# Kernel tuning notes

Measured on AMD Instinct MI355X. Metric: run time of the kernel, lower is better.

The kernel has to match this reference:

```python
import jax, jax.numpy as jnp
import numpy as np

NUM_BINS = 256          # CLAHE histogram bins (kornia default)
GRID = (8, 8)           # CLAHE tile grid (kornia default)
LOG_GAIN = 2.5          # module init arg
CLIP_LIMIT = 1.0        # module init arg


def normalize_in_range(x, lo=0.0, hi=1.0):
    mn = x.min()
    mx = x.max()
    return (x - mn) / (mx - mn) * (hi - lo) + lo


def adjust_log(x, gain):
    # skimage/kornia log adjust: gain * log2(1 + x)
    return gain * jnp.log2(1.0 + x)


def equalize_clahe(x, clip_limit=CLIP_LIMIT, grid=GRID):
    B, C, H, W = x.shape
    gh, gw = grid
    th = -(-H // gh)   # ceil tile height
    tw = -(-W // gw)   # ceil tile width
    Hp, Wp = th * gh, tw * gw
    if (Hp, Wp) != (H, W):
        x = jnp.pad(x, ((0, 0), (0, 0), (0, Hp - H), (0, Wp - W)), mode='reflect')

    # bin index per pixel (values saturated into [0,1])
    xc = jnp.clip(x, 0.0, 1.0)
    bins = jnp.clip((xc * NUM_BINS).astype(jnp.int32), 0, NUM_BINS - 1)  # B,C,Hp,Wp

    # --- per-tile histograms: (B*C*gh*gw) tiles of th*tw pixels ---
    tb = bins.reshape(B, C, gh, th, gw, tw).transpose(0, 1, 2, 4, 3, 5)
    tb = tb.reshape(B * C * gh * gw, th * tw)
    hist = jax.vmap(lambda ix: jnp.bincount(ix, length=NUM_BINS))(tb).astype(jnp.float32)

    pixels = th * tw
    # --- clip + uniform redistribution of excess ---
    if clip_limit > 0:
        clip_max = max(int(clip_limit * pixels // NUM_BINS), 1)
        excess = jnp.maximum(hist - clip_max, 0.0).sum(-1)
        hist = jnp.minimum(hist, float(clip_max))
        redist = jnp.floor(excess / NUM_BINS)
        residual = excess - redist * NUM_BINS
        hist = hist + redist[:, None] \
             + (jnp.arange(NUM_BINS)[None, :] < residual[:, None]).astype(hist.dtype)

    # --- CDF -> LUT in [0, 255] ---
    lut = jnp.clip(jnp.floor(jnp.cumsum(hist, -1) * ((NUM_BINS - 1) / pixels)), 0.0, NUM_BINS - 1.0)
    lut = lut.reshape(B, C, gh, gw, NUM_BINS)

    # --- bilinear interpolation between the 4 neighboring tile LUTs ---
    iy = jnp.arange(Hp, dtype=jnp.float32)
    ty = (iy + 0.5) / th - 0.5
    y0f = jnp.floor(ty)
    wy = (ty - y0f)[:, None]                                   # Hp x 1
    y0 = jnp.clip(y0f.astype(jnp.int32), 0, gh - 1)[:, None]
    y1 = jnp.clip(y0f.astype(jnp.int32) + 1, 0, gh - 1)[:, None]

    ix = jnp.arange(Wp, dtype=jnp.float32)
    tx = (ix + 0.5) / tw - 0.5
    x0f = jnp.floor(tx)
    wx = (tx - x0f)[None, :]
    x0 = jnp.clip(x0f.astype(jnp.int32), 0, gw - 1)[None, :]
    x1 = jnp.clip(x0f.astype(jnp.int32) + 1, 0, gw - 1)[None, :]

    flat_lut = lut.reshape(-1)
    bidx = jnp.arange(B)[:, None, None, None]
    cidx = jnp.arange(C)[None, :, None, None]

    def gather(yi, xi):
        idx = (((bidx * C + cidx) * gh + yi) * gw + xi) * NUM_BINS + bins
        return flat_lut[idx]

    v = (1.0 - wy) * ((1.0 - wx) * gather(y0, x0) + wx * gather(y0, x1)) \
        + wy * ((1.0 - wx) * gather(y1, x0) + wx * gather(y1, x1))
    out = v / (NUM_BINS - 1)
    return out[..., :H, :W]


def setup_inputs() -> dict:
    key = jax.random.key(0)
    x = jax.random.uniform(key, (8, 1, 2048, 2048), dtype=jnp.float32)
    return {"x": x}


def reference(x):
    shape = x.shape
    x = normalize_in_range(x, 0.0, 1.0)
    x = adjust_log(x, gain=LOG_GAIN)
    x = equalize_clahe(x, clip_limit=CLIP_LIMIT)
    x = normalize_in_range(x, 0.0, 1.0)
    return x.reshape(shape)
```

## Files before the change

### kernel.cpp

```cpp
#include <hip/hip_runtime.h>

#define NIMG 8
#define IMH 2048
#define IMW 2048
#define GH 8
#define GW 8
#define NBINS 256
#define NTPI 64
#define CLIP_MAXF 256.0f
#define LUT_SCALE 0.0038909912109375f
#define LOG_GAIN_F 2.5f

#define MM_BLOCKS 2048
#define APPLY_BLOCKS (16 * 16 * NIMG)

__device__ __forceinline__ int pix_bin(float v, float mn, float den) {
    float xn = (v - mn) / den;
    float t  = LOG_GAIN_F * log2f(1.0f + xn);
    float xc = fminf(fmaxf(t, 0.0f), 1.0f);
    int b = (int)(xc * 256.0f);
    return min(max(b, 0), 255);
}

__device__ __forceinline__ void mm4(float4 v, float& mn, float& mx) {
    mn = fminf(mn, fminf(fminf(v.x, v.y), fminf(v.z, v.w)));
    mx = fmaxf(mx, fmaxf(fmaxf(v.x, v.y), fmaxf(v.z, v.w)));
}

template <int NWAVES>
__device__ __forceinline__ void block_minmax_all(float& mn, float& mx, int t) {
#pragma unroll
    for (int m = 32; m >= 1; m >>= 1) {
        mn = fminf(mn, __shfl_xor(mn, m, 64));
        mx = fmaxf(mx, __shfl_xor(mx, m, 64));
    }
    __shared__ float smn[NWAVES], smx[NWAVES];
    int wid = t >> 6, lid = t & 63;
    if (lid == 0) { smn[wid] = mn; smx[wid] = mx; }
    __syncthreads();
    mn = smn[0]; mx = smx[0];
#pragma unroll
    for (int i = 1; i < NWAVES; i++) { mn = fminf(mn, smn[i]); mx = fmaxf(mx, smx[i]); }
}

__global__ __launch_bounds__(256) void k_minmax_in(const float4* __restrict__ x,
                                                   float2* __restrict__ red) {
    int t = threadIdx.x;
    size_t base = (size_t)blockIdx.x * 4096 + t;
    float mn = 3.4e38f, mx = -3.4e38f;
#pragma unroll
    for (int k = 0; k < 16; k += 4) {
        float4 v0 = x[base + (size_t)(k + 0) * 256];
        float4 v1 = x[base + (size_t)(k + 1) * 256];
        float4 v2 = x[base + (size_t)(k + 2) * 256];
        float4 v3 = x[base + (size_t)(k + 3) * 256];
        mm4(v0, mn, mx); mm4(v1, mn, mx); mm4(v2, mn, mx); mm4(v3, mn, mx);
    }
    block_minmax_all<4>(mn, mx, t);
    if (t == 0) red[blockIdx.x] = make_float2(mn, mx);
}

__global__ __launch_bounds__(256) void k_reduce_minmax(const float2* __restrict__ red, int n,
                                                       float* __restrict__ sc, int slot) {
    int t = threadIdx.x;
    float mn = 3.4e38f, mx = -3.4e38f;
    for (int i = t; i < n; i += 256) {
        float2 p = red[i];
        mn = fminf(mn, p.x);
        mx = fmaxf(mx, p.y);
    }
    block_minmax_all<4>(mn, mx, t);
    if (t == 0) { sc[slot] = mn; sc[slot + 1] = mx; }
}

template <bool STOREBINS>
__global__ __launch_bounds__(1024) void k_hist(const float* __restrict__ x,
                                               const float2* __restrict__ red1,
                                               float* __restrict__ lut,
                                               uchar4* __restrict__ bins) {
    int t = threadIdx.x;

    float mn, mx;
    {
        float2 p0 = red1[t];
        float2 p1 = red1[t + 1024];
        mn = fminf(p0.x, p1.x);
        mx = fmaxf(p0.y, p1.y);
        block_minmax_all<16>(mn, mx, t);
    }
    float den = mx - mn;

    __shared__ unsigned sh[NBINS];
    if (t < NBINS) sh[t] = 0u;
    __syncthreads();

    int tile = blockIdx.x;
    int img  = blockIdx.y;
    int ty = tile >> 3, tx = tile & 7;

    size_t base = ((size_t)img * IMH + (size_t)ty * 256) * IMW + (size_t)tx * 256;
    const float* xt = x + base;
    int lid = t & 63;
    int rowoff = t >> 6;
    int c4 = t & 63;

    for (int it = 0; it < 16; ++it) {
        int r = (it << 4) + rowoff;
        float4 v = *(const float4*)(xt + (size_t)r * IMW + (c4 << 2));
        int b[4];
        b[0] = pix_bin(v.x, mn, den);
        b[1] = pix_bin(v.y, mn, den);
        b[2] = pix_bin(v.z, mn, den);
        b[3] = pix_bin(v.w, mn, den);
#pragma unroll
        for (int j = 0; j < 4; j++) {
            bool hot = (b[j] == 255);
            unsigned long long m = __ballot(hot);
            if (!hot) atomicAdd(&sh[b[j]], 1u);
            if (lid == 0 && m) atomicAdd(&sh[255], (unsigned)__popcll(m));
        }
        if (STOREBINS) {
            uchar4 q;
            q.x = (unsigned char)b[0]; q.y = (unsigned char)b[1];
            q.z = (unsigned char)b[2]; q.w = (unsigned char)b[3];
            bins[(base + (size_t)r * IMW + (size_t)(c4 << 2)) >> 2] = q;
        }
    }
    __syncthreads();

    int wid = t >> 6;
    float h = 0.0f, ex = 0.0f;
    if (t < NBINS) {
        h = (float)sh[t];
        ex = fmaxf(h - CLIP_MAXF, 0.0f);
    }
    float s = ex;
#pragma unroll
    for (int m = 1; m < 64; m <<= 1) s += __shfl_xor(s, m, 64);
    __shared__ float wpart[16];
    if (lid == 0) wpart[wid] = s;
    __syncthreads();
    float excess = wpart[0] + wpart[1] + wpart[2] + wpart[3];

    h = fminf(h, CLIP_MAXF);
    float redist   = floorf(excess * (1.0f / 256.0f));
    float residual = excess - redist * 256.0f;
    h = h + redist + (((float)t < residual) ? 1.0f : 0.0f);

    float c = h;
#pragma unroll
    for (int m = 1; m < 64; m <<= 1) {
        float o = __shfl_up(c, m, 64);
        if (lid >= m) c += o;
    }
    __shared__ float wsum[16];
    if (lid == 63) wsum[wid] = c;
    __syncthreads();
    if (t < NBINS) {
        float off = 0.0f;
        for (int i = 0; i < wid; i++) off += wsum[i];
        c += off;
        float l = fminf(floorf(c * LUT_SCALE), 255.0f);
        l = fmaxf(l, 0.0f);
        lut[((size_t)img * NTPI + tile) * NBINS + t] = l;
    }
}

template <bool USE_BINS, bool FINAL>
__global__ __launch_bounds__(256) void k_apply(const uchar4* __restrict__ bins,
                                               const float* __restrict__ x,
                                               const float* __restrict__ lut,
                                               const float* __restrict__ sc,
                                               float2* __restrict__ red2,
                                               float4* __restrict__ out) {
    __shared__ float L[4][NBINS];
    int t = threadIdx.x;

    float pmn = 0.f, oscale = 1.f;
    if (FINAL) {
        float vmn = 3.4e38f, vmx = -3.4e38f;
#pragma unroll
        for (int k = 0; k < 8; k++) {
            float2 p = red2[t + k * 256];
            vmn = fminf(vmn, p.x);
            vmx = fmaxf(vmx, p.y);
        }
        block_minmax_all<4>(vmn, vmx, t);
        pmn = vmn * (1.0f / 255.0f);
        float pmx = vmx * (1.0f / 255.0f);
        oscale = 1.0f / (pmx - pmn);
    }

    int qx = blockIdx.x, qy = blockIdx.y, img = blockIdx.z;
    int ty = qy >> 1, tx = qx >> 1;
    int yA = (qy & 1) ? ty : max(ty - 1, 0);
    int yB = (qy & 1) ? min(ty + 1, GH - 1) : ty;
    int xA = (qx & 1) ? tx : max(tx - 1, 0);
    int xB = (qx & 1) ? min(tx + 1, GW - 1) : tx;

    const float* lb = lut + (size_t)img * NTPI * NBINS;
    L[0][t] = lb[(size_t)(yA * GW + xA) * NBINS + t];
    L[1][t] = lb[(size_t)(yA * GW + xB) * NBINS + t];
    L[2][t] = lb[(size_t)(yB * GW + xA) * NBINS + t];
    L[3][t] = lb[(size_t)(yB * GW + xB) * NBINS + t];
    __syncthreads();

    float mn = 0.f, den = 1.f;
    if (!USE_BINS) { mn = sc[0]; den = sc[1] - mn; }

    float vmnl = 3.4e38f, vmxl = -3.4e38f;
    int gy0 = qy << 7, gx0 = qx << 7;
    int rowoff = t >> 5;
    int c4 = t & 31;

    for (int it = 0; it < 16; ++it) {
        int r = (it << 3) + rowoff;
        int iy = gy0 + r;
        int ix0 = gx0 + (c4 << 2);
        size_t pidx = ((size_t)img * IMH + iy) * IMW + ix0;

        int b[4];
        if (USE_BINS) {
            uchar4 q = bins[pidx >> 2];
            b[0] = q.x; b[1] = q.y; b[2] = q.z; b[3] = q.w;
        } else {
            float4 v = *(const float4*)(x + pidx);
            b[0] = pix_bin(v.x, mn, den);
            b[1] = pix_bin(v.y, mn, den);
            b[2] = pix_bin(v.z, mn, den);
            b[3] = pix_bin(v.w, mn, den);
        }

        float tyf = ((float)iy + 0.5f) * (1.0f / 256.0f) - 0.5f;
        float wy = tyf - floorf(tyf);
        float4 o;
        float* op = &o.x;
#pragma unroll
        for (int j = 0; j < 4; j++) {
            float txf = ((float)(ix0 + j) + 0.5f) * (1.0f / 256.0f) - 0.5f;
            float wx = txf - floorf(txf);
            float g00 = L[0][b[j]], g01 = L[1][b[j]];
            float g10 = L[2][b[j]], g11 = L[3][b[j]];
            float v = (1.0f - wy) * ((1.0f - wx) * g00 + wx * g01) +
                      wy * ((1.0f - wx) * g10 + wx * g11);
            if (FINAL) {
                float p = v * (1.0f / 255.0f);
                op[j] = (p - pmn) * oscale;
            } else {
                vmnl = fminf(vmnl, v);
                vmxl = fmaxf(vmxl, v);
            }
        }
        if (FINAL) out[pidx >> 2] = o;
    }

    if (!FINAL) {
        block_minmax_all<4>(vmnl, vmxl, t);
        if (t == 0) {
            int bid = (img * 16 + qy) * 16 + qx;
            red2[bid] = make_float2(vmnl, vmxl);
        }
    }
}

extern "C" void kernel_launch(void* const* d_in, const int* in_sizes, int n_in,
                              void* d_out, int out_size, void* d_ws, size_t ws_size,
                              hipStream_t stream) {
    const float* x = (const float*)d_in[0];
    float4* out = (float4*)d_out;

    unsigned char* ws = (unsigned char*)d_ws;
    float* sc     = (float*)ws;
    float* lut    = (float*)(ws + 64);
    float2* red1  = (float2*)(ws + 64 + 512 * 1024);
    float2* red2  = (float2*)(ws + 64 + 512 * 1024 + 16384);
    uchar4* bins  = (uchar4*)(ws + 1024 * 1024);

    size_t need_bins = 1024 * 1024 + (size_t)NIMG * IMH * IMW;
    bool use_bins = (ws_size >= need_bins);

    k_minmax_in<<<dim3(MM_BLOCKS), dim3(256), 0, stream>>>((const float4*)x, red1);

    dim3 qgrid(16, 16, NIMG);
    if (use_bins) {
        k_hist<true><<<dim3(NTPI, NIMG), dim3(1024), 0, stream>>>(x, red1, lut, bins);
        k_apply<true, false><<<qgrid, dim3(256), 0, stream>>>(bins, x, lut, sc, red2, out);
        k_apply<true, true><<<qgrid, dim3(256), 0, stream>>>(bins, x, lut, sc, red2, out);
    } else {
        k_reduce_minmax<<<dim3(1), dim3(256), 0, stream>>>(red1, MM_BLOCKS, sc, 0);
        k_hist<false><<<dim3(NTPI, NIMG), dim3(1024), 0, stream>>>(x, red1, lut, bins);
        k_apply<false, false><<<qgrid, dim3(256), 0, stream>>>(bins, x, lut, sc, red2, out);
        k_apply<false, true><<<qgrid, dim3(256), 0, stream>>>(bins, x, lut, sc, red2, out);
    }
}
```

Measured before the change: 121.4 us.

## Fuse CLAHE pipeline into one cooperative kernel with grid syncs and LDS bins

Replaces the four-kernel sequence (min/max, histogram+LUT, apply-minmax, apply-final) with one cooperative kernel of 512 blocks, one per tile, separated by grid-wide syncs. Each block keeps its tile's 256x256 bin indices in 64KB of shared memory, so the global bins buffer is neither written nor read twice and launch gaps disappear. In exchange it needs co-residency of all 512 blocks of 512 threads with 64KB+ LDS each, which may not fit and falls back to the multi-kernel path. The fallback's k_apply now loads L twice, with an out-of-range write when t>=256 in a 256-thread block.

```diff
diff --git a/kernel.cpp b/kernel.cpp
--- a/kernel.cpp
+++ b/kernel.cpp
@@ -1,4 +1,7 @@
 #include <hip/hip_runtime.h>
+#include <hip/hip_cooperative_groups.h>
+
+namespace cg = cooperative_groups;
 
 #define NIMG 8
 #define IMH 2048
@@ -11,8 +14,8 @@
 #define LUT_SCALE 0.0038909912109375f
 #define LOG_GAIN_F 2.5f
 
+#define FUSED_BLOCKS 512
 #define MM_BLOCKS 2048
-#define APPLY_BLOCKS (16 * 16 * NIMG)
 
 __device__ __forceinline__ int pix_bin(float v, float mn, float den) {
     float xn = (v - mn) / den;
@@ -29,12 +32,13 @@
 
 template <int NWAVES>
 __device__ __forceinline__ void block_minmax_all(float& mn, float& mx, int t) {
+    __shared__ float smn[NWAVES], smx[NWAVES];
+    __syncthreads();
 #pragma unroll
     for (int m = 32; m >= 1; m >>= 1) {
         mn = fminf(mn, __shfl_xor(mn, m, 64));
         mx = fmaxf(mx, __shfl_xor(mx, m, 64));
     }
-    __shared__ float smn[NWAVES], smx[NWAVES];
     int wid = t >> 6, lid = t & 63;
     if (lid == 0) { smn[wid] = mn; smx[wid] = mx; }
     __syncthreads();
@@ -42,6 +46,207 @@
 #pragma unroll
     for (int i = 1; i < NWAVES; i++) { mn = fminf(mn, smn[i]); mx = fmaxf(mx, smx[i]); }
 }
+
+__device__ __forceinline__ void load_L(const float* __restrict__ lb, int qy, int qx,
+                                       float (*L)[NBINS], int t) {
+    int ty = qy >> 1, tx = qx >> 1;
+    int yA = (qy & 1) ? ty : max(ty - 1, 0);
+    int yB = (qy & 1) ? min(ty + 1, GH - 1) : ty;
+    int xA = (qx & 1) ? tx : max(tx - 1, 0);
+    int xB = (qx & 1) ? min(tx + 1, GW - 1) : tx;
+    int ci = t & 255;
+#pragma unroll
+    for (int j = 0; j < 2; ++j) {
+        int which = (t >> 8) + 2 * j;
+        int yy = (which >= 2) ? yB : yA;
+        int xx = (which & 1) ? xB : xA;
+        L[which][ci] = lb[(size_t)(yy * GW + xx) * NBINS + ci];
+    }
+}
+
+__global__ __launch_bounds__(512, 4) void k_fused(const float* __restrict__ x,
+                                                  float2* __restrict__ red1,
+                                                  float2* __restrict__ red2,
+                                                  float* __restrict__ lutg,
+                                                  float4* __restrict__ out) {
+    cg::grid_group gridg = cg::this_grid();
+    __shared__ unsigned char binsL[256 * 256];
+    __shared__ float L[4][NBINS];
+    __shared__ unsigned sh[NBINS];
+
+    int t = threadIdx.x;
+    int bid = blockIdx.x;
+    int img = bid >> 6, tile = bid & 63;
+    int ty = tile >> 3, tx = tile & 7;
+
+    float mn = 3.4e38f, mx = -3.4e38f;
+    {
+        const float4* x4 = (const float4*)x;
+        size_t base = (size_t)bid * 16384 + t;
+#pragma unroll
+        for (int k = 0; k < 32; k += 4) {
+            float4 v0 = x4[base + (size_t)(k + 0) * 512];
+            float4 v1 = x4[base + (size_t)(k + 1) * 512];
+            float4 v2 = x4[base + (size_t)(k + 2) * 512];
+            float4 v3 = x4[base + (size_t)(k + 3) * 512];
+            mm4(v0, mn, mx); mm4(v1, mn, mx); mm4(v2, mn, mx); mm4(v3, mn, mx);
+        }
+        block_minmax_all<8>(mn, mx, t);
+        if (t == 0) red1[bid] = make_float2(mn, mx);
+    }
+    gridg.sync();
+
+    {
+        float2 p = red1[t];
+        mn = p.x; mx = p.y;
+        block_minmax_all<8>(mn, mx, t);
+    }
+    float den = mx - mn;
+
+    if (t < NBINS) sh[t] = 0u;
+    __syncthreads();
+
+    size_t tbase = ((size_t)img * IMH + (size_t)ty * 256) * IMW + (size_t)tx * 256;
+    int lid = t & 63;
+    {
+        int rowoff = t >> 6;
+        int c4 = t & 63;
+        for (int it = 0; it < 32; ++it) {
+            int r = (it << 3) + rowoff;
+            float4 v = *(const float4*)(x + tbase + (size_t)r * IMW + (c4 << 2));
+            int b[4];
+            b[0] = pix_bin(v.x, mn, den);
+            b[1] = pix_bin(v.y, mn, den);
+            b[2] = pix_bin(v.z, mn, den);
+            b[3] = pix_bin(v.w, mn, den);
+#pragma unroll
+            for (int j = 0; j < 4; j++) {
+                bool hot = (b[j] == 255);
+                unsigned long long m = __ballot(hot);
+                if (!hot) atomicAdd(&sh[b[j]], 1u);
+                if (lid == 0 && m) atomicAdd(&sh[255], (unsigned)__popcll(m));
+            }
+            uchar4 q;
+            q.x = (unsigned char)b[0]; q.y = (unsigned char)b[1];
+            q.z = (unsigned char)b[2]; q.w = (unsigned char)b[3];
+            ((uchar4*)binsL)[(r << 6) + c4] = q;
+        }
+    }
+    __syncthreads();
+
+    {
+        int wid = t >> 6;
+        float h = 0.0f, ex = 0.0f;
+        if (t < NBINS) {
+            h = (float)sh[t];
+            ex = fmaxf(h - CLIP_MAXF, 0.0f);
+        }
+        float s = ex;
+#pragma unroll
+        for (int m = 1; m < 64; m <<= 1) s += __shfl_xor(s, m, 64);
+        __shared__ float wpart[8];
+        if (lid == 0) wpart[wid] = s;
+        __syncthreads();
+        float excess = wpart[0] + wpart[1] + wpart[2] + wpart[3];
+
+        h = fminf(h, CLIP_MAXF);
+        float redist   = floorf(excess * (1.0f / 256.0f));
+        float residual = excess - redist * 256.0f;
+        h = h + redist + (((float)t < residual) ? 1.0f : 0.0f);
+
+        float c = h;
+#pragma unroll
+        for (int m = 1; m < 64; m <<= 1) {
+            float o = __shfl_up(c, m, 64);
+            if (lid >= m) c += o;
+        }
+        __shared__ float wsum[8];
+        if (lid == 63) wsum[wid] = c;
+        __syncthreads();
+        if (t < NBINS) {
+            float off = 0.0f;
+            for (int i = 0; i < wid; i++) off += wsum[i];
+            c += off;
+            float l = fminf(floorf(c * LUT_SCALE), 255.0f);
+            l = fmaxf(l, 0.0f);
+            lutg[((size_t)img * NTPI + tile) * NBINS + t] = l;
+        }
+    }
+    gridg.sync();
+
+    const float* lb = lutg + (size_t)img * NTPI * NBINS;
+    float vmn = 3.4e38f, vmx = -3.4e38f;
+    for (int q = 0; q < 4; ++q) {
+        int qy = (ty << 1) + (q >> 1), qx = (tx << 1) + (q & 1);
+        __syncthreads();
+        load_L(lb, qy, qx, L, t);
+        __syncthreads();
+        int ly0 = (q >> 1) << 7, lx0 = (q & 1) << 7;
+        int rowoff = t >> 5, col4 = t & 31;
+        for (int it = 0; it < 8; ++it) {
+            int r = (it << 4) + rowoff;
+            uchar4 qb = ((const uchar4*)binsL)[((ly0 + r) << 6) + (lx0 >> 2) + col4];
+            int iy = (ty << 8) + ly0 + r;
+            float tyf = ((float)iy + 0.5f) * (1.0f / 256.0f) - 0.5f;
+            float wy = tyf - floorf(tyf);
+            int ix0 = (tx << 8) + lx0 + (col4 << 2);
+            int b[4] = {qb.x, qb.y, qb.z, qb.w};
+#pragma unroll
+            for (int j = 0; j < 4; j++) {
+                float txf = ((float)(ix0 + j) + 0.5f) * (1.0f / 256.0f) - 0.5f;
+                float wx = txf - floorf(txf);
+                float v = (1.0f - wy) * ((1.0f - wx) * L[0][b[j]] + wx * L[1][b[j]]) +
+                          wy * ((1.0f - wx) * L[2][b[j]] + wx * L[3][b[j]]);
+                vmn = fminf(vmn, v);
+                vmx = fmaxf(vmx, v);
+            }
+        }
+    }
+    block_minmax_all<8>(vmn, vmx, t);
+    if (t == 0) red2[bid] = make_float2(vmn, vmx);
+    gridg.sync();
+
+    float pmn, oscale;
+    {
+        float2 p = red2[t];
+        float a = p.x, b2 = p.y;
+        block_minmax_all<8>(a, b2, t);
+        pmn = a * (1.0f / 255.0f);
+        float pmx = b2 * (1.0f / 255.0f);
+        oscale = 1.0f / (pmx - pmn);
+    }
+    for (int q = 0; q < 4; ++q) {
+        int qy = (ty << 1) + (q >> 1), qx = (tx << 1) + (q & 1);
+        __syncthreads();
+        load_L(lb, qy, qx, L, t);
+        __syncthreads();
+        int ly0 = (q >> 1) << 7, lx0 = (q & 1) << 7;
+        int rowoff = t >> 5, col4 = t & 31;
+        for (int it = 0; it < 8; ++it) {
+            int r = (it << 4) + rowoff;
+            uchar4 qb = ((const uchar4*)binsL)[((ly0 + r) << 6) + (lx0 >> 2) + col4];
+            int iy = (ty << 8) + ly0 + r;
+            float tyf = ((float)iy + 0.5f) * (1.0f / 256.0f) - 0.5f;
+            float wy = tyf - floorf(tyf);
+            int ix0 = (tx << 8) + lx0 + (col4 << 2);
+            int b[4] = {qb.x, qb.y, qb.z, qb.w};
+            float4 o;
+            float* op = &o.x;
+#pragma unroll
+            for (int j = 0; j < 4; j++) {
+                float txf = ((float)(ix0 + j) + 0.5f) * (1.0f / 256.0f) - 0.5f;
+                float wx = txf - floorf(txf);
+                float v = (1.0f - wy) * ((1.0f - wx) * L[0][b[j]] + wx * L[1][b[j]]) +
+                          wy * ((1.0f - wx) * L[2][b[j]] + wx * L[3][b[j]]);
+                float p = v * (1.0f / 255.0f);
+                op[j] = (p - pmn) * oscale;
+            }
+            size_t pidx = ((size_t)img * IMH + iy) * IMW + ix0;
+            out[pidx >> 2] = o;
+        }
+    }
+}
+
 
 __global__ __launch_bounds__(256) void k_minmax_in(const float4* __restrict__ x,
                                                    float2* __restrict__ red) {
@@ -60,26 +265,11 @@
     if (t == 0) red[blockIdx.x] = make_float2(mn, mx);
 }
 
-__global__ __launch_bounds__(256) void k_reduce_minmax(const float2* __restrict__ red, int n,
-                                                       float* __restrict__ sc, int slot) {
-    int t = threadIdx.x;
-    float mn = 3.4e38f, mx = -3.4e38f;
-    for (int i = t; i < n; i += 256) {
-        float2 p = red[i];
-        mn = fminf(mn, p.x);
-        mx = fmaxf(mx, p.y);
-    }
-    block_minmax_all<4>(mn, mx, t);
-    if (t == 0) { sc[slot] = mn; sc[slot + 1] = mx; }
-}
-
-template <bool STOREBINS>
 __global__ __launch_bounds__(1024) void k_hist(const float* __restrict__ x,
                                                const float2* __restrict__ red1,
                                                float* __restrict__ lut,
                                                uchar4* __restrict__ bins) {
     int t = threadIdx.x;
-
     float mn, mx;
     {
         float2 p0 = red1[t];
@@ -97,7 +287,6 @@
     int tile = blockIdx.x;
     int img  = blockIdx.y;
     int ty = tile >> 3, tx = tile & 7;
-
     size_t base = ((size_t)img * IMH + (size_t)ty * 256) * IMW + (size_t)tx * 256;
     const float* xt = x + base;
     int lid = t & 63;
@@ -119,12 +308,10 @@
             if (!hot) atomicAdd(&sh[b[j]], 1u);
             if (lid == 0 && m) atomicAdd(&sh[255], (unsigned)__popcll(m));
         }
-        if (STOREBINS) {
-            uchar4 q;
-            q.x = (unsigned char)b[0]; q.y = (unsigned char)b[1];
-            q.z = (unsigned char)b[2]; q.w = (unsigned char)b[3];
-            bins[(base + (size_t)r * IMW + (size_t)(c4 << 2)) >> 2] = q;
-        }
+        uchar4 q;
+        q.x = (unsigned char)b[0]; q.y = (unsigned char)b[1];
+        q.z = (unsigned char)b[2]; q.w = (unsigned char)b[3];
+        bins[(base + (size_t)r * IMW + (size_t)(c4 << 2)) >> 2] = q;
     }
     __syncthreads();
 
@@ -166,11 +353,9 @@
     }
 }
 
-template <bool USE_BINS, bool FINAL>
+template <bool FINAL>
 __global__ __launch_bounds__(256) void k_apply(const uchar4* __restrict__ bins,
-                                               const float* __restrict__ x,
                                                const float* __restrict__ lut,
-                                               const float* __restrict__ sc,
                                                float2* __restrict__ red2,
                                                float4* __restrict__ out) {
     __shared__ float L[4][NBINS];
@@ -192,21 +377,21 @@
     }
 
     int qx = blockIdx.x, qy = blockIdx.y, img = blockIdx.z;
-    int ty = qy >> 1, tx = qx >> 1;
-    int yA = (qy & 1) ? ty : max(ty - 1, 0);
-    int yB = (qy & 1) ? min(ty + 1, GH - 1) : ty;
-    int xA = (qx & 1) ? tx : max(tx - 1, 0);
-    int xB = (qx & 1) ? min(tx + 1, GW - 1) : tx;
-
     const float* lb = lut + (size_t)img * NTPI * NBINS;
-    L[0][t] = lb[(size_t)(yA * GW + xA) * NBINS + t];
-    L[1][t] = lb[(size_t)(yA * GW + xB) * NBINS + t];
-    L[2][t] = lb[(size_t)(yB * GW + xA) * NBINS + t];
-    L[3][t] = lb[(size_t)(yB * GW + xB) * NBINS + t];
-    __syncthreads();
-
-    float mn = 0.f, den = 1.f;
-    if (!USE_BINS) { mn = sc[0]; den = sc[1] - mn; }
+    load_L(lb, qy, qx, L, t | ((t >> 8) << 8));
+    {
+        int ci = t & 255;
+        int ty2 = qy >> 1, tx2 = qx >> 1;
+        int yA = (qy & 1) ? ty2 : max(ty2 - 1, 0);
+        int yB = (qy & 1) ? min(ty2 + 1, GH - 1) : ty2;
+        int xA = (qx & 1) ? tx2 : max(tx2 - 1, 0);
+        int xB = (qx & 1) ? min(tx2 + 1, GW - 1) : tx2;
+        L[0][ci] = lb[(size_t)(yA * GW + xA) * NBINS + ci];
+        L[1][ci] = lb[(size_t)(yA * GW + xB) * NBINS + ci];
+        L[2][ci] = lb[(size_t)(yB * GW + xA) * NBINS + ci];
+        L[3][ci] = lb[(size_t)(yB * GW + xB) * NBINS + ci];
+    }
+    __syncthreads();
 
     float vmnl = 3.4e38f, vmxl = -3.4e38f;
     int gy0 = qy << 7, gx0 = qx << 7;
@@ -218,18 +403,8 @@
         int iy = gy0 + r;
         int ix0 = gx0 + (c4 << 2);
         size_t pidx = ((size_t)img * IMH + iy) * IMW + ix0;
-
-        int b[4];
-        if (USE_BINS) {
-            uchar4 q = bins[pidx >> 2];
-            b[0] = q.x; b[1] = q.y; b[2] = q.z; b[3] = q.w;
-        } else {
-            float4 v = *(const float4*)(x + pidx);
-            b[0] = pix_bin(v.x, mn, den);
-            b[1] = pix_bin(v.y, mn, den);
-            b[2] = pix_bin(v.z, mn, den);
-            b[3] = pix_bin(v.w, mn, den);
-        }
+        uchar4 q = bins[pidx >> 2];
+        int b[4] = {q.x, q.y, q.z, q.w};
 
         float tyf = ((float)iy + 0.5f) * (1.0f / 256.0f) - 0.5f;
         float wy = tyf - floorf(tyf);
@@ -239,10 +414,8 @@
         for (int j = 0; j < 4; j++) {
             float txf = ((float)(ix0 + j) + 0.5f) * (1.0f / 256.0f) - 0.5f;
             float wx = txf - floorf(txf);
-            float g00 = L[0][b[j]], g01 = L[1][b[j]];
-            float g10 = L[2][b[j]], g11 = L[3][b[j]];
-            float v = (1.0f - wy) * ((1.0f - wx) * g00 + wx * g01) +
-                      wy * ((1.0f - wx) * g10 + wx * g11);
+            float v = (1.0f - wy) * ((1.0f - wx) * L[0][b[j]] + wx * L[1][b[j]]) +
+                      wy * ((1.0f - wx) * L[2][b[j]] + wx * L[3][b[j]]);
             if (FINAL) {
                 float p = v * (1.0f / 255.0f);
                 op[j] = (p - pmn) * oscale;
@@ -270,26 +443,23 @@
     float4* out = (float4*)d_out;
 
     unsigned char* ws = (unsigned char*)d_ws;
-    float* sc     = (float*)ws;
     float* lut    = (float*)(ws + 64);
     float2* red1  = (float2*)(ws + 64 + 512 * 1024);
     float2* red2  = (float2*)(ws + 64 + 512 * 1024 + 16384);
     uchar4* bins  = (uchar4*)(ws + 1024 * 1024);
 
-    size_t need_bins = 1024 * 1024 + (size_t)NIMG * IMH * IMW;
-    bool use_bins = (ws_size >= need_bins);
+    {
+        void* args[] = {(void*)&x, (void*)&red1, (void*)&red2, (void*)&lut, (void*)&out};
+        hipError_t e = hipLaunchCooperativeKernel((const void*)k_fused,
+                                                  dim3(FUSED_BLOCKS), dim3(512),
+                                                  args, 0, stream);
+        if (e == hipSuccess) return;
+        (void)hipGetLastError();
+    }
 
     k_minmax_in<<<dim3(MM_BLOCKS), dim3(256), 0, stream>>>((const float4*)x, red1);
-
+    k_hist<<<dim3(NTPI, NIMG), dim3(1024), 0, stream>>>(x, red1, lut, bins);
     dim3 qgrid(16, 16, NIMG);
-    if (use_bins) {
-        k_hist<true><<<dim3(NTPI, NIMG), dim3(1024), 0, stream>>>(x, red1, lut, bins);
-        k_apply<true, false><<<qgrid, dim3(256), 0, stream>>>(bins, x, lut, sc, red2, out);
-        k_apply<true, true><<<qgrid, dim3(256), 0, stream>>>(bins, x, lut, sc, red2, out);
-    } else {
-        k_reduce_minmax<<<dim3(1), dim3(256), 0, stream>>>(red1, MM_BLOCKS, sc, 0);
-        k_hist<false><<<dim3(NTPI, NIMG), dim3(1024), 0, stream>>>(x, red1, lut, bins);
-        k_apply<false, false><<<qgrid, dim3(256), 0, stream>>>(bins, x, lut, sc, red2, out);
-        k_apply<false, true><<<qgrid, dim3(256), 0, stream>>>(bins, x, lut, sc, red2, out);
-    }
-}
+    k_apply<false><<<qgrid, dim3(256), 0, stream>>>(bins, lut, red2, out);
+    k_apply<true><<<qgrid, dim3(256), 0, stream>>>(bins, lut, red2, out);
+}
```

Measured after the change: 276.9 us. 128% more time.
